# Kernel optimization log

Hardware: AMD Instinct MI355X
Metric: run time of the kernel (lower is better)

The kernel has to match this reference:

```python
import jax, jax.numpy as jnp
import numpy as np

HEADS = 8

def setup_inputs() -> dict:
    key = jax.random.key(0)
    ks = jax.random.split(key, 6)
    b, c, h, w = 32, 64, 56, 56
    m, dim = 6, 192
    inner = HEADS * c  # 512
    return {
        "x": jax.random.normal(ks[0], (b, c, h, w), dtype=jnp.float32),
        "z": jax.random.normal(ks[1], (b, m, dim), dtype=jnp.float32),
        "Wq": jax.random.normal(ks[2], (inner, dim), dtype=jnp.float32) * 0.05,
        "bq": jax.random.normal(ks[3], (inner,), dtype=jnp.float32) * 0.05,
        "Wo": jax.random.normal(ks[4], (dim, inner), dtype=jnp.float32) * 0.05,
        "bo": jax.random.normal(ks[5], (dim,), dtype=jnp.float32) * 0.05,
    }

def reference(x, z, Wq, bq, Wo, bo):
    b, c, h, w = x.shape
    _, m, d = z.shape
    heads = HEADS
    scale = d ** (-0.5)
    # torch: x.view(b, h*w, c) on contiguous (b,c,h,w) == plain reshape (memory reinterpretation)
    xf = x.reshape(b, h * w, c)
    # torch: repeat(1,1,heads) then view(b, heads, h*w, c) -- exact reshape semantics
    kv = jnp.tile(xf, (1, 1, heads)).reshape(b, heads, h * w, c)  # K = V
    # torch Linear: z @ Wq.T + bq, then view(b, heads, m, c)
    q = (jnp.einsum('bmd,id->bmi', z, Wq) + bq).reshape(b, heads, m, c)
    dots = jnp.einsum('bhmc,bhlc->bhml', q, kv) * scale
    attn = jax.nn.softmax(dots, axis=-1)
    out = jnp.einsum('bhml,bhlc->bhmc', attn, kv)
    out = out.transpose(0, 2, 1, 3).reshape(b, m, heads * c)  # 'b h m c -> b m (h c)'
    return z + jnp.einsum('bmi,di->bmd', out, Wo) + bo
```

## Files before the change

kernel.cpp:

```cpp
#include <hip/hip_runtime.h>
#include <math.h>

#define BATCH 32
#define NHEADS 8
#define M 6
#define DIM 192
#define CDIM 64
#define INNER 512
#define LFULL 3136
#define RDIST 392
#define EPITCH 400
#define NT 1024
#define KCHUNKS 98

__global__ __launch_bounds__(NT) void fused_kernel(const float* __restrict__ x,
                                                   const float* __restrict__ z,
                                                   const float* __restrict__ Wq,
                                                   const float* __restrict__ bq,
                                                   const float* __restrict__ Wo,
                                                   const float* __restrict__ bo,
                                                   float* __restrict__ out) {
    __shared__ float sK[RDIST * CDIM];
    __shared__ float sQ[M * CDIM];
    __shared__ float sE[M][EPITCH];
    __shared__ float sPart[16][M * CDIM];
    __shared__ float sInv[M];
    __shared__ float sO[M * CDIM];

    const int b   = blockIdx.x >> 3;
    const int hh  = blockIdx.x & (NHEADS - 1);
    const int tid = threadIdx.x;
    const int wave = tid >> 6;
    const int lane = tid & 63;
    const int sub  = lane & 15;
    const int grp  = lane >> 4;

    const float* K = x + (size_t)b * (LFULL * CDIM) + (size_t)hh * (RDIST * CDIM);

    {
        const char* Kb = (const char*)K;
        for (int c = wave; c < KCHUNKS; c += 16) {
            int L = (c << 10) + (lane << 4);
            int G = L ^ ((((unsigned)L >> 8) & 15) << 4);
            __builtin_amdgcn_global_load_lds(
                (const __attribute__((address_space(1))) void*)(Kb + G),
                (__attribute__((address_space(3))) void*)((char*)sK + (c << 10)),
                16, 0, 0);
        }
    }

    {
        const float4* Wq4 = (const float4*)Wq;
        const float4* zb4 = (const float4*)(z + (size_t)b * (M * DIM));
        const float inv_sqrt = rsqrtf((float)DIM);
        #pragma unroll
        for (int t = 0; t < 6; ++t) {
            int o  = ((wave * 6 + t) << 2) | grp;
            int gi = hh * (M * CDIM) + o;
            int iz = gi & (INNER - 1);
            int mz = gi >> 9;
            const float4* wr = Wq4 + (size_t)iz * (DIM / 4);
            const float4* zr = zb4 + (size_t)mz * (DIM / 4);
            float acc = 0.f;
            #pragma unroll
            for (int k2 = 0; k2 < 3; ++k2) {
                float4 wv = wr[sub + 16 * k2];
                float4 zv = zr[sub + 16 * k2];
                acc += wv.x * zv.x + wv.y * zv.y + wv.z * zv.z + wv.w * zv.w;
            }
            acc += __shfl_xor(acc, 1);
            acc += __shfl_xor(acc, 2);
            acc += __shfl_xor(acc, 4);
            acc += __shfl_xor(acc, 8);
            if (sub == 0) sQ[o] = (acc + bq[iz]) * inv_sqrt;
        }
    }
    asm volatile("s_waitcnt vmcnt(0)" ::: "memory");
    __syncthreads();

    if (tid < 2 * RDIST) {
        const int r  = tid >> 1;
        const int hf = tid & 1;
        const float4* sK4 = (const float4*)sK;
        const float4* q4  = (const float4*)sQ;
        float d[M] = {0, 0, 0, 0, 0, 0};
        #pragma unroll
        for (int j = 0; j < 8; ++j) {
            int s = hf * 8 + j;
            float4 k4 = sK4[(r << 4) + (s ^ (r & 15))];
            #pragma unroll
            for (int mm = 0; mm < M; ++mm) {
                float4 qv = q4[mm * (CDIM / 4) + s];
                d[mm] += k4.x * qv.x + k4.y * qv.y + k4.z * qv.z + k4.w * qv.w;
            }
        }
        #pragma unroll
        for (int mm = 0; mm < M; ++mm) {
            float tot = d[mm] + __shfl_xor(d[mm], 1);
            if (!hf) sE[mm][r] = __expf(tot);
        }
    }
    __syncthreads();

    if (wave < M) {
        float s = (lane < RDIST - 384) ? sE[wave][384 + lane] : 0.f;
        #pragma unroll
        for (int k = 0; k < 6; ++k) s += sE[wave][lane + 64 * k];
        #pragma unroll
        for (int off = 32; off; off >>= 1) s += __shfl_xor(s, off);
        if (lane == 0) sInv[wave] = 1.0f / s;
    }

    {
        float acc[M] = {0, 0, 0, 0, 0, 0};
        for (int r = wave; r < RDIST; r += 16) {
            float kv = sK[(r << 6) + (lane ^ ((r & 15) << 2))];
            #pragma unroll
            for (int mm = 0; mm < M; ++mm) acc[mm] += sE[mm][r] * kv;
        }
        #pragma unroll
        for (int mm = 0; mm < M; ++mm) sPart[wave][mm * CDIM + lane] = acc[mm];
    }
    __syncthreads();

    if (tid < M * CDIM) {
        float v = 0.f;
        #pragma unroll
        for (int g = 0; g < 16; ++g) v += sPart[g][tid];
        sO[tid] = v * sInv[tid >> 6];
    }
    __syncthreads();

    {
        const float4* Wo4 = (const float4*)Wo;
        const float4* sO4 = (const float4*)sO;
        const int hc04 = hh * (CDIM / 4);
        #pragma unroll
        for (int t = 0; t < 3; ++t) {
            int slot = wave * 3 + t + hh * 6;
            if (slot >= 48) slot -= 48;
            int dd = (slot << 2) | grp;
            float4 wv = Wo4[(size_t)dd * (INNER / 4) + hc04 + sub];
            #pragma unroll
            for (int mm = 0; mm < M; ++mm) {
                float4 s4 = sO4[mm * (CDIM / 4) + sub];
                float p = wv.x * s4.x + wv.y * s4.y + wv.z * s4.z + wv.w * s4.w;
                p += __shfl_xor(p, 1);
                p += __shfl_xor(p, 2);
                p += __shfl_xor(p, 4);
                p += __shfl_xor(p, 8);
                if (sub == mm) {
                    int oi = mm * DIM + dd;
                    float v = p;
                    if (hh == 0) v += z[(size_t)b * (M * DIM) + oi] + bo[dd];
                    atomicAdd(out + (size_t)b * (M * DIM) + oi, v);
                }
            }
        }
    }
}

extern "C" void kernel_launch(void* const* d_in, const int* in_sizes, int n_in,
                              void* d_out, int out_size, void* d_ws, size_t ws_size,
                              hipStream_t stream) {
    const float* x  = (const float*)d_in[0];
    const float* z  = (const float*)d_in[1];
    const float* Wq = (const float*)d_in[2];
    const float* bq = (const float*)d_in[3];
    const float* Wo = (const float*)d_in[4];
    const float* bo = (const float*)d_in[5];
    float* out = (float*)d_out;

    fused_kernel<<<BATCH * NHEADS, NT, 0, stream>>>(x, z, Wq, bq, Wo, bo, out);
}
```

Measured before the change: 122.7 us.

## Split output projection into separate kernel, removing atomic accumulation

The per-head attention kernel now writes its normalized output into a workspace buffer and no longer runs the output projection. A second kernel loads each batch's full 6x512 attention output into shared memory and computes the Wo projection with plain stores, adding z and bo once. This removes the atomicAdd traffic and the reliance on a pre-zeroed output buffer, and frees shared memory in the main kernel. The cost is an extra kernel launch and a round trip through global memory for the intermediate.

```diff
diff --git a/kernel.cpp b/kernel.cpp
--- a/kernel.cpp
+++ b/kernel.cpp
@@ -12,20 +12,18 @@
 #define EPITCH 400
 #define NT 1024
 #define KCHUNKS 98
+#define WS_FLOATS (BATCH * M * INNER)
 
 __global__ __launch_bounds__(NT) void fused_kernel(const float* __restrict__ x,
                                                    const float* __restrict__ z,
                                                    const float* __restrict__ Wq,
                                                    const float* __restrict__ bq,
-                                                   const float* __restrict__ Wo,
-                                                   const float* __restrict__ bo,
-                                                   float* __restrict__ out) {
+                                                   float* __restrict__ ws) {
     __shared__ float sK[RDIST * CDIM];
     __shared__ float sQ[M * CDIM];
     __shared__ float sE[M][EPITCH];
     __shared__ float sPart[16][M * CDIM];
     __shared__ float sInv[M];
-    __shared__ float sO[M * CDIM];
 
     const int b   = blockIdx.x >> 3;
     const int hh  = blockIdx.x & (NHEADS - 1);
@@ -127,34 +125,57 @@
         float v = 0.f;
         #pragma unroll
         for (int g = 0; g < 16; ++g) v += sPart[g][tid];
-        sO[tid] = v * sInv[tid >> 6];
+        v *= sInv[tid >> 6];
+        const int mm = tid >> 6;
+        const int c  = tid & 63;
+        ws[(size_t)(b * M + mm) * INNER + hh * CDIM + c] = v;
+    }
+}
+
+__global__ __launch_bounds__(256) void oproj_kernel(const float* __restrict__ ws,
+                                                    const float* __restrict__ z,
+                                                    const float* __restrict__ Wo,
+                                                    const float* __restrict__ bo,
+                                                    float* __restrict__ out) {
+    __shared__ float sW[M * INNER];
+    const int bb  = blockIdx.x / 6;
+    const int dg  = blockIdx.x % 6;
+    const int tid = threadIdx.x;
+
+    {
+        const float4* ws4 = (const float4*)(ws + (size_t)bb * (M * INNER));
+        float4* sW4w = (float4*)sW;
+        #pragma unroll
+        for (int t = 0; t < 3; ++t) sW4w[tid + 256 * t] = ws4[tid + 256 * t];
     }
     __syncthreads();
 
-    {
-        const float4* Wo4 = (const float4*)Wo;
-        const float4* sO4 = (const float4*)sO;
-        const int hc04 = hh * (CDIM / 4);
+    const int g   = tid >> 4;
+    const int sub = tid & 15;
+    const float4* sW4 = (const float4*)sW;
+    #pragma unroll
+    for (int pass = 0; pass < 2; ++pass) {
+        const int d = dg * 32 + pass * 16 + g;
+        const float4* wo4 = (const float4*)Wo + (size_t)d * (INNER / 4);
+        float4 wv[8];
         #pragma unroll
-        for (int t = 0; t < 3; ++t) {
-            int slot = wave * 3 + t + hh * 6;
-            if (slot >= 48) slot -= 48;
-            int dd = (slot << 2) | grp;
-            float4 wv = Wo4[(size_t)dd * (INNER / 4) + hc04 + sub];
+        for (int kk = 0; kk < 8; ++kk) wv[kk] = wo4[sub + 16 * kk];
+        #pragma unroll
+        for (int mm = 0; mm < M; ++mm) {
+            float acc = 0.f;
             #pragma unroll
-            for (int mm = 0; mm < M; ++mm) {
-                float4 s4 = sO4[mm * (CDIM / 4) + sub];
-                float p = wv.x * s4.x + wv.y * s4.y + wv.z * s4.z + wv.w * s4.w;
-                p += __shfl_xor(p, 1);
-                p += __shfl_xor(p, 2);
-                p += __shfl_xor(p, 4);
-                p += __shfl_xor(p, 8);
-                if (sub == mm) {
-                    int oi = mm * DIM + dd;
-                    float v = p;
-                    if (hh == 0) v += z[(size_t)b * (M * DIM) + oi] + bo[dd];
-                    atomicAdd(out + (size_t)b * (M * DIM) + oi, v);
-                }
+            for (int kk = 0; kk < 8; ++kk) {
+                float4 s4 = sW4[mm * (INNER / 4) + sub + 16 * kk];
+                acc += wv[kk].x * s4.x + wv[kk].y * s4.y + wv[kk].z * s4.z + wv[kk].w * s4.w;
+            }
+            acc += __shfl_xor(acc, 1);
+            acc += __shfl_xor(acc, 2);
+            acc += __shfl_xor(acc, 4);
+            acc += __shfl_xor(acc, 8);
+            if (sub == mm) {
+                const int oi = mm * DIM + d;
+                out[(size_t)bb * (M * DIM) + oi] =
+                    acc + z[(size_t)bb * (M * DIM) + oi] + bo[d];
             }
         }
     }
@@ -170,6 +191,8 @@
     const float* Wo = (const float*)d_in[4];
     const float* bo = (const float*)d_in[5];
     float* out = (float*)d_out;
+    float* ws  = (float*)d_ws;
 
-    fused_kernel<<<BATCH * NHEADS, NT, 0, stream>>>(x, z, Wq, bq, Wo, bo, out);
+    fused_kernel<<<BATCH * NHEADS, NT, 0, stream>>>(x, z, Wq, bq, ws);
+    oproj_kernel<<<BATCH * M, 256, 0, stream>>>(ws, z, Wo, bo, out);
 }
```

Result: faster. 120.2 us (-2.1%).

## Split query rows across two blocks and read K directly from global memory

Applied to the files above, without the earlier changes.

The grid doubles so each block handles half of the six query rows for one batch-head pair. The big shared-memory staging of K through global_load_lds is dropped, and both QK dots and the AV accumulation now read K straight from global memory, relying on L2 and cache hits for the second pass. This cuts shared memory per block to allow more resident blocks and more parallelism, at the cost of reading K twice per block and twice across the two blocks per head.

```diff
diff --git a/kernel.cpp b/kernel.cpp
--- a/kernel.cpp
+++ b/kernel.cpp
@@ -4,6 +4,7 @@
 #define BATCH 32
 #define NHEADS 8
 #define M 6
+#define MH 3
 #define DIM 192
 #define CDIM 64
 #define INNER 512
@@ -11,149 +12,135 @@
 #define RDIST 392
 #define EPITCH 400
 #define NT 1024
-#define KCHUNKS 98
 
-__global__ __launch_bounds__(NT) void fused_kernel(const float* __restrict__ x,
-                                                   const float* __restrict__ z,
-                                                   const float* __restrict__ Wq,
-                                                   const float* __restrict__ bq,
-                                                   const float* __restrict__ Wo,
-                                                   const float* __restrict__ bo,
-                                                   float* __restrict__ out) {
-    __shared__ float sK[RDIST * CDIM];
-    __shared__ float sQ[M * CDIM];
-    __shared__ float sE[M][EPITCH];
-    __shared__ float sPart[16][M * CDIM];
-    __shared__ float sInv[M];
-    __shared__ float sO[M * CDIM];
+__global__ __launch_bounds__(NT, 8) void attn_kernel(const float* __restrict__ x,
+                                                     const float* __restrict__ z,
+                                                     const float* __restrict__ Wq,
+                                                     const float* __restrict__ bq,
+                                                     const float* __restrict__ Wo,
+                                                     const float* __restrict__ bo,
+                                                     float* __restrict__ out) {
+    __shared__ float sQ[MH * CDIM];
+    __shared__ float sE[MH][EPITCH];
+    __shared__ float sPart[8][MH * CDIM];
+    __shared__ float sO[MH * CDIM];
+    __shared__ float sInv[MH];
 
-    const int b   = blockIdx.x >> 3;
-    const int hh  = blockIdx.x & (NHEADS - 1);
-    const int tid = threadIdx.x;
+    const int bid = blockIdx.x;
+    const int b   = bid & 31;
+    const int hh  = (bid >> 5) & 7;
+    const int mh  = bid >> 8;
+    const int tid  = threadIdx.x;
     const int wave = tid >> 6;
     const int lane = tid & 63;
     const int sub  = lane & 15;
     const int grp  = lane >> 4;
+    const int g    = (wave << 2) | grp;
 
     const float* K = x + (size_t)b * (LFULL * CDIM) + (size_t)hh * (RDIST * CDIM);
 
     {
-        const char* Kb = (const char*)K;
-        for (int c = wave; c < KCHUNKS; c += 16) {
-            int L = (c << 10) + (lane << 4);
-            int G = L ^ ((((unsigned)L >> 8) & 15) << 4);
-            __builtin_amdgcn_global_load_lds(
-                (const __attribute__((address_space(1))) void*)(Kb + G),
-                (__attribute__((address_space(3))) void*)((char*)sK + (c << 10)),
-                16, 0, 0);
-        }
-    }
-
-    {
-        const float4* Wq4 = (const float4*)Wq;
-        const float4* zb4 = (const float4*)(z + (size_t)b * (M * DIM));
         const float inv_sqrt = rsqrtf((float)DIM);
         #pragma unroll
-        for (int t = 0; t < 6; ++t) {
-            int o  = ((wave * 6 + t) << 2) | grp;
-            int gi = hh * (M * CDIM) + o;
-            int iz = gi & (INNER - 1);
-            int mz = gi >> 9;
-            const float4* wr = Wq4 + (size_t)iz * (DIM / 4);
-            const float4* zr = zb4 + (size_t)mz * (DIM / 4);
-            float acc = 0.f;
-            #pragma unroll
-            for (int k2 = 0; k2 < 3; ++k2) {
-                float4 wv = wr[sub + 16 * k2];
-                float4 zv = zr[sub + 16 * k2];
-                acc += wv.x * zv.x + wv.y * zv.y + wv.z * zv.z + wv.w * zv.w;
-            }
+        for (int t = 0; t < MH; ++t) {
+            const int flat = hh * (M * CDIM) + (mh * MH + t) * CDIM + g;
+            const int iz = flat & (INNER - 1);
+            const int mz = flat >> 9;
+            const float4* wr = (const float4*)(Wq + (size_t)iz * DIM);
+            const float4* zr = (const float4*)(z + (size_t)(b * M + mz) * DIM);
+            float4 w0 = wr[sub], w1 = wr[sub + 16], w2 = wr[sub + 32];
+            float4 z0 = zr[sub], z1 = zr[sub + 16], z2 = zr[sub + 32];
+            float acc = w0.x * z0.x + w0.y * z0.y + w0.z * z0.z + w0.w * z0.w
+                      + w1.x * z1.x + w1.y * z1.y + w1.z * z1.z + w1.w * z1.w
+                      + w2.x * z2.x + w2.y * z2.y + w2.z * z2.z + w2.w * z2.w;
             acc += __shfl_xor(acc, 1);
             acc += __shfl_xor(acc, 2);
             acc += __shfl_xor(acc, 4);
             acc += __shfl_xor(acc, 8);
-            if (sub == 0) sQ[o] = (acc + bq[iz]) * inv_sqrt;
+            if (sub == 0) sQ[t * CDIM + g] = (acc + bq[iz]) * inv_sqrt;
         }
     }
-    asm volatile("s_waitcnt vmcnt(0)" ::: "memory");
     __syncthreads();
 
     if (tid < 2 * RDIST) {
         const int r  = tid >> 1;
         const int hf = tid & 1;
-        const float4* sK4 = (const float4*)sK;
-        const float4* q4  = (const float4*)sQ;
-        float d[M] = {0, 0, 0, 0, 0, 0};
+        const float4* kr = (const float4*)(K + (size_t)r * CDIM) + (hf << 3);
+        const float4* q4 = (const float4*)sQ;
+        float d0 = 0.f, d1 = 0.f, d2 = 0.f;
         #pragma unroll
         for (int j = 0; j < 8; ++j) {
-            int s = hf * 8 + j;
-            float4 k4 = sK4[(r << 4) + (s ^ (r & 15))];
-            #pragma unroll
-            for (int mm = 0; mm < M; ++mm) {
-                float4 qv = q4[mm * (CDIM / 4) + s];
-                d[mm] += k4.x * qv.x + k4.y * qv.y + k4.z * qv.z + k4.w * qv.w;
-            }
+            float4 k4 = kr[j];
+            const int s = (hf << 3) + j;
+            float4 q0 = q4[s], q1 = q4[16 + s], q2 = q4[32 + s];
+            d0 += k4.x * q0.x + k4.y * q0.y + k4.z * q0.z + k4.w * q0.w;
+            d1 += k4.x * q1.x + k4.y * q1.y + k4.z * q1.z + k4.w * q1.w;
+            d2 += k4.x * q2.x + k4.y * q2.y + k4.z * q2.z + k4.w * q2.w;
         }
-        #pragma unroll
-        for (int mm = 0; mm < M; ++mm) {
-            float tot = d[mm] + __shfl_xor(d[mm], 1);
-            if (!hf) sE[mm][r] = __expf(tot);
+        d0 += __shfl_xor(d0, 1);
+        d1 += __shfl_xor(d1, 1);
+        d2 += __shfl_xor(d2, 1);
+        if (!hf) {
+            sE[0][r] = __expf(d0);
+            sE[1][r] = __expf(d1);
+            sE[2][r] = __expf(d2);
         }
     }
     __syncthreads();
 
-    if (wave < M) {
-        float s = (lane < RDIST - 384) ? sE[wave][384 + lane] : 0.f;
+    if (wave >= 8 && wave < 8 + MH) {
+        const int m = wave - 8;
+        float s = (lane < RDIST - 384) ? sE[m][384 + lane] : 0.f;
         #pragma unroll
-        for (int k = 0; k < 6; ++k) s += sE[wave][lane + 64 * k];
+        for (int k = 0; k < 6; ++k) s += sE[m][lane + (k << 6)];
         #pragma unroll
         for (int off = 32; off; off >>= 1) s += __shfl_xor(s, off);
-        if (lane == 0) sInv[wave] = 1.0f / s;
+        if (lane == 0) sInv[m] = 1.0f / s;
     }
 
-    {
-        float acc[M] = {0, 0, 0, 0, 0, 0};
-        for (int r = wave; r < RDIST; r += 16) {
-            float kv = sK[(r << 6) + (lane ^ ((r & 15) << 2))];
-            #pragma unroll
-            for (int mm = 0; mm < M; ++mm) acc[mm] += sE[mm][r] * kv;
+    if (wave < 8) {
+        float a0 = 0.f, a1 = 0.f, a2 = 0.f;
+        for (int r = wave; r < RDIST; r += 8) {
+            float kv = K[((size_t)r << 6) + lane];
+            float e0 = sE[0][r], e1 = sE[1][r], e2 = sE[2][r];
+            a0 += e0 * kv; a1 += e1 * kv; a2 += e2 * kv;
         }
-        #pragma unroll
-        for (int mm = 0; mm < M; ++mm) sPart[wave][mm * CDIM + lane] = acc[mm];
+        sPart[wave][lane]            = a0;
+        sPart[wave][CDIM + lane]     = a1;
+        sPart[wave][2 * CDIM + lane] = a2;
     }
     __syncthreads();
 
-    if (tid < M * CDIM) {
+    if (tid < MH * CDIM) {
         float v = 0.f;
         #pragma unroll
-        for (int g = 0; g < 16; ++g) v += sPart[g][tid];
+        for (int gg = 0; gg < 8; ++gg) v += sPart[gg][tid];
         sO[tid] = v * sInv[tid >> 6];
     }
     __syncthreads();
 
     {
-        const float4* Wo4 = (const float4*)Wo;
-        const float4* sO4 = (const float4*)sO;
-        const int hc04 = hh * (CDIM / 4);
         #pragma unroll
-        for (int t = 0; t < 3; ++t) {
-            int slot = wave * 3 + t + hh * 6;
-            if (slot >= 48) slot -= 48;
-            int dd = (slot << 2) | grp;
-            float4 wv = Wo4[(size_t)dd * (INNER / 4) + hc04 + sub];
+        for (int t = 0; t < MH; ++t) {
+            int d = g * 3 + t + hh * 24;
+            if (d >= DIM) d -= DIM;
+            const float4* wo4 = (const float4*)(Wo + (size_t)d * INNER + hh * CDIM);
+            float4 wv = wo4[sub];
             #pragma unroll
-            for (int mm = 0; mm < M; ++mm) {
-                float4 s4 = sO4[mm * (CDIM / 4) + sub];
+            for (int mm = 0; mm < MH; ++mm) {
+                const float4* so4 = (const float4*)(sO + mm * CDIM);
+                float4 s4 = so4[sub];
                 float p = wv.x * s4.x + wv.y * s4.y + wv.z * s4.z + wv.w * s4.w;
                 p += __shfl_xor(p, 1);
                 p += __shfl_xor(p, 2);
                 p += __shfl_xor(p, 4);
                 p += __shfl_xor(p, 8);
                 if (sub == mm) {
-                    int oi = mm * DIM + dd;
+                    const int mg = mh * MH + mm;
+                    const size_t oi = (size_t)b * (M * DIM) + mg * DIM + d;
                     float v = p;
-                    if (hh == 0) v += z[(size_t)b * (M * DIM) + oi] + bo[dd];
-                    atomicAdd(out + (size_t)b * (M * DIM) + oi, v);
+                    if (hh == 0) v += z[oi] + bo[d];
+                    atomicAdd(out + oi, v);
                 }
             }
         }
@@ -171,5 +158,5 @@
     const float* bo = (const float*)d_in[5];
     float* out = (float*)d_out;
 
-    fused_kernel<<<BATCH * NHEADS, NT, 0, stream>>>(x, z, Wq, bq, Wo, bo, out);
+    attn_kernel<<<BATCH * NHEADS * 2, NT, 0, stream>>>(x, z, Wq, bq, Wo, bo, out);
 }
```

After: 104.6 us. 1.17x faster.
